# Performance work log

Measured on AMD Instinct MI355X. Metric: run time of the kernel, lower is better.

The kernel has to match this reference:

```python
import jax, jax.numpy as jnp
import numpy as np

N, E = 50000, 800000
IN_DIM, HID, OUT, HEADS = 128, 128, 64, 4
C1 = HID // HEADS  # 32 per-head channels in gat1
NEG_SLOPE = 0.2


def _gat_conv(x, src, dst, W, a_src, a_dst, b, heads, ch):
    """PyG GATConv (inference): gather -> edge attention -> segment softmax -> scatter."""
    n = x.shape[0]
    h = (x @ W).reshape(n, heads, ch)                      # [N,H,C]
    alpha_src = jnp.einsum('nhc,hc->nh', h, a_src)         # [N,H]
    alpha_dst = jnp.einsum('nhc,hc->nh', h, a_dst)         # [N,H]
    e = jax.nn.leaky_relu(alpha_src[src] + alpha_dst[dst], NEG_SLOPE)  # [E,H]
    m = jax.ops.segment_max(e, dst, num_segments=n)        # per-target max (stable softmax)
    e = jnp.exp(e - m[dst])
    denom = jax.ops.segment_sum(e, dst, num_segments=n)
    alpha = e / (denom[dst] + 1e-16)                       # [E,H]
    out = jax.ops.segment_sum(h[src] * alpha[:, :, None], dst, num_segments=n)  # [N,H,C]
    return out.reshape(n, heads * ch) + b


def setup_inputs() -> dict:
    key = jax.random.key(0)
    ks = jax.random.split(key, 16)
    x = jax.random.normal(ks[0], (N, IN_DIM), dtype=jnp.float32)
    edge_index = jax.random.randint(ks[1], (2, E), 0, N, dtype=jnp.int64)
    s = lambda fan_in: 1.0 / np.sqrt(fan_in)
    return {
        'x': x,
        'edge_index': edge_index,
        'W1': jax.random.normal(ks[2], (IN_DIM, HEADS * C1), jnp.float32) * s(IN_DIM),
        'a_src1': jax.random.normal(ks[3], (HEADS, C1), jnp.float32) * s(C1),
        'a_dst1': jax.random.normal(ks[4], (HEADS, C1), jnp.float32) * s(C1),
        'b1': jnp.zeros((HID,), jnp.float32),
        'W2': jax.random.normal(ks[5], (HID, OUT), jnp.float32) * s(HID),
        'a_src2': jax.random.normal(ks[6], (1, OUT), jnp.float32) * s(OUT),
        'a_dst2': jax.random.normal(ks[7], (1, OUT), jnp.float32) * s(OUT),
        'b2': jnp.zeros((OUT,), jnp.float32),
        'pw1': jax.random.normal(ks[8], (OUT, OUT), jnp.float32) * s(OUT),
        'pb1': jnp.zeros((OUT,), jnp.float32),
        'pw2': jax.random.normal(ks[9], (OUT, OUT), jnp.float32) * s(OUT),
        'pb2': jnp.zeros((OUT,), jnp.float32),
    }


def reference(x, edge_index, W1, a_src1, a_dst1, b1, W2, a_src2, a_dst2, b2, pw1, pb1, pw2, pb2):
    n = x.shape[0]
    # PyG GATConv add_self_loops=True
    loops = jnp.arange(n, dtype=edge_index.dtype)
    src = jnp.concatenate([edge_index[0], loops])
    dst = jnp.concatenate([edge_index[1], loops])
    h = jax.nn.elu(_gat_conv(x, src, dst, W1, a_src1, a_dst1, b1, HEADS, C1))
    h = jax.nn.elu(_gat_conv(h, src, dst, W2, a_src2, a_dst2, b2, 1, OUT))
    # origin_proj: Linear -> ReLU -> Linear
    h = jax.nn.relu(h @ pw1 + pb1)
    return h @ pw2 + pb2
```

## Files before the change

### kernel.cpp

```cpp
#include <hip/hip_runtime.h>
#include <math.h>

#define N_NODES 50000
#define N_EDGES 800000
#define ET (N_EDGES + N_NODES)
#define IN_DIM 128
#define HID 128
#define OUT_DIM 64
#define BW 64
#define NBUCK ((N_NODES + BW - 1) / BW)
#define NBLK 256
#define EPB 3328

__device__ __forceinline__ float lrelu(float x){ return x >= 0.f ? x : 0.2f * x; }
__device__ __forceinline__ float eluf(float x){ return x > 0.f ? x : expm1f(x); }
__device__ __forceinline__ unsigned f2bf(float f){
    unsigned u = __float_as_uint(f);
    return (u + 0x7fffu + ((u >> 16) & 1u)) >> 16;
}
__device__ __forceinline__ float bflo(unsigned u){ return __uint_as_float(u << 16); }
__device__ __forceinline__ float bfhi(unsigned u){ return __uint_as_float(u & 0xffff0000u); }

__global__ __launch_bounds__(256) void k_count(const int* __restrict__ dst, int* __restrict__ C)
{
    __shared__ int cnt[NBUCK];
    const int tid = threadIdx.x, blk = blockIdx.x;
    for (int i = tid; i < NBUCK; i += 256) cnt[i] = 0;
    __syncthreads();
    #pragma unroll
    for (int j = 0; j < EPB / 256; j++) {
        const int e = blk * EPB + j * 256 + tid;
        if (e < ET) {
            const int d = (e < N_EDGES) ? dst[e] : (e - N_EDGES);
            atomicAdd(&cnt[d >> 6], 1);
        }
    }
    __syncthreads();
    for (int b = tid; b < NBUCK; b += 256) C[b * NBLK + blk] = cnt[b];
}

__global__ __launch_bounds__(256) void k_bsumA(const int* __restrict__ C, int* __restrict__ bsum2)
{
    __shared__ int red[4];
    int v = C[blockIdx.x * NBLK + threadIdx.x];
    #pragma unroll
    for (int off = 32; off > 0; off >>= 1) v += __shfl_down(v, off);
    if ((threadIdx.x & 63) == 0) red[threadIdx.x >> 6] = v;
    __syncthreads();
    if (threadIdx.x == 0) bsum2[blockIdx.x] = red[0] + red[1] + red[2] + red[3];
}

__global__ __launch_bounds__(1024) void k_bscanB(const int* __restrict__ bsum2, int* __restrict__ boff2)
{
    __shared__ int part[1024];
    const int t = threadIdx.x;
    int v = (t < NBUCK) ? bsum2[t] : 0;
    part[t] = v;
    __syncthreads();
    #pragma unroll
    for (int d = 1; d < 1024; d <<= 1) {
        int add = (t >= d) ? part[t - d] : 0;
        __syncthreads();
        part[t] += add;
        __syncthreads();
    }
    if (t < NBUCK) boff2[t] = part[t] - v;
    if (t == 0) boff2[NBUCK] = ET;
}

__global__ __launch_bounds__(256) void k_cscanC(const int* __restrict__ C,
                                                const int* __restrict__ boff2,
                                                int* __restrict__ Cs)
{
    __shared__ int part[256];
    const int t = threadIdx.x, b = blockIdx.x;
    int v = C[b * NBLK + t];
    part[t] = v;
    __syncthreads();
    #pragma unroll
    for (int d = 1; d < 256; d <<= 1) {
        int add = (t >= d) ? part[t - d] : 0;
        __syncthreads();
        part[t] += add;
        __syncthreads();
    }
    Cs[b * NBLK + t] = boff2[b] + part[t] - v;
}

__global__ __launch_bounds__(256) void k_part2(const int* __restrict__ src,
                                               const int* __restrict__ dst,
                                               const int* __restrict__ Cs,
                                               uint2* __restrict__ part)
{
    __shared__ int base[NBUCK];
    __shared__ int cnt[NBUCK];
    const int tid = threadIdx.x, blk = blockIdx.x;
    for (int b = tid; b < NBUCK; b += 256) { base[b] = Cs[b * NBLK + blk]; cnt[b] = 0; }
    __syncthreads();
    #pragma unroll
    for (int j = 0; j < EPB / 256; j++) {
        const int e = blk * EPB + j * 256 + tid;
        if (e < ET) {
            int s, d;
            if (e < N_EDGES) { s = src[e]; d = dst[e]; } else { s = d = e - N_EDGES; }
            const int b = d >> 6;
            const int r = atomicAdd(&cnt[b], 1);
            part[base[b] + r] = make_uint2((unsigned)d, (unsigned)s);
        }
    }
}

__global__ __launch_bounds__(256) void k_scat2(const int* __restrict__ boff2,
                                               const uint2* __restrict__ part,
                                               int* __restrict__ rowptr,
                                               int* __restrict__ csr_src)
{
    __shared__ int cnt64[BW];
    __shared__ int nbase[BW];
    const int b = blockIdx.x, tid = threadIdx.x;
    const int n0 = b * BW;
    const int lo = boff2[b], hi = boff2[b + 1];
    if (tid < BW) cnt64[tid] = 0;
    __syncthreads();
    for (int i = lo + tid; i < hi; i += 256) {
        atomicAdd(&cnt64[part[i].x & (BW - 1)], 1);
    }
    __syncthreads();
    if (tid < BW) {
        int v = cnt64[tid];
        int incl = v;
        #pragma unroll
        for (int off = 1; off < 64; off <<= 1) {
            int t2 = __shfl_up(incl, off);
            if (tid >= off) incl += t2;
        }
        const int excl = incl - v;
        nbase[tid] = excl;
        const int n = n0 + tid;
        if (n < N_NODES) rowptr[n] = lo + excl;
        cnt64[tid] = 0;
    }
    if (b == 0 && tid == 0) rowptr[N_NODES] = ET;
    __syncthreads();
    for (int i = lo + tid; i < hi; i += 256) {
        const uint2 p = part[i];
        const int dn = (int)p.x & (BW - 1);
        const int r = atomicAdd(&cnt64[dn], 1);
        csr_src[lo + nbase[dn] + r] = (int)p.y;
    }
}

__global__ __launch_bounds__(256, 2) void k_gemm1(
    const float* __restrict__ x, const float* __restrict__ W1,
    const float* __restrict__ a_s, const float* __restrict__ a_d,
    unsigned* __restrict__ h1b, float* __restrict__ as1, float* __restrict__ ad1)
{
    __shared__ float sW[128 * 128];
    __shared__ float sx[32][128];
    const int tid = threadIdx.x;
    for (int i = tid; i < 4096; i += 256) ((float4*)sW)[i] = ((const float4*)W1)[i];
    const int cg = tid & 31;
    const int ng = tid >> 5;
    const float4 as4 = ((const float4*)a_s)[cg];
    const float4 ad4 = ((const float4*)a_d)[cg];
    const int nGroups = (N_NODES + 31) / 32;
    for (int g = blockIdx.x; g < nGroups; g += gridDim.x) {
        const int n0 = g * 32;
        __syncthreads();
        #pragma unroll
        for (int j = 0; j < 4; j++) {
            const int i = tid + 256 * j;
            const int node = i >> 5, quad = i & 31;
            const int n = n0 + node;
            float4 v = make_float4(0.f, 0.f, 0.f, 0.f);
            if (n < N_NODES) v = ((const float4*)x)[n * 32 + quad];
            *(float4*)&sx[node][4 * quad] = v;
        }
        __syncthreads();
        float4 acc[4];
        #pragma unroll
        for (int m = 0; m < 4; m++) acc[m] = make_float4(0.f, 0.f, 0.f, 0.f);
        #pragma unroll 8
        for (int k = 0; k < 128; k++) {
            const float4 w = *(const float4*)&sW[k * 128 + 4 * cg];
            #pragma unroll
            for (int m = 0; m < 4; m++) {
                const float xv = sx[4 * ng + m][k];
                acc[m].x = fmaf(xv, w.x, acc[m].x);
                acc[m].y = fmaf(xv, w.y, acc[m].y);
                acc[m].z = fmaf(xv, w.z, acc[m].z);
                acc[m].w = fmaf(xv, w.w, acc[m].w);
            }
        }
        #pragma unroll
        for (int m = 0; m < 4; m++) {
            const int n = n0 + 4 * ng + m;
            float ps = acc[m].x * as4.x + acc[m].y * as4.y + acc[m].z * as4.z + acc[m].w * as4.w;
            float pd = acc[m].x * ad4.x + acc[m].y * ad4.y + acc[m].z * ad4.z + acc[m].w * ad4.w;
            #pragma unroll
            for (int off = 1; off < 8; off <<= 1) {
                ps += __shfl_xor(ps, off);
                pd += __shfl_xor(pd, off);
            }
            if (n < N_NODES) {
                uint2 pk;
                pk.x = f2bf(acc[m].x) | (f2bf(acc[m].y) << 16);
                pk.y = f2bf(acc[m].z) | (f2bf(acc[m].w) << 16);
                ((uint2*)h1b)[n * 32 + cg] = pk;
                if ((cg & 7) == 0) {
                    as1[n * 4 + (cg >> 3)] = ps;
                    ad1[n * 4 + (cg >> 3)] = pd;
                }
            }
        }
    }
}

__global__ __launch_bounds__(256) void k_aggr1(
    const int* __restrict__ rowptr, const int* __restrict__ csr_src,
    const float* __restrict__ as1, const float* __restrict__ ad1,
    const uint4* __restrict__ h1u4, float* __restrict__ acc1)
{
    const int d  = blockIdx.x * 16 + (threadIdx.x >> 4);
    const int c8 = threadIdx.x & 15;
    const int hd = c8 >> 2;
    const int r0 = rowptr[d], r1 = rowptr[d + 1];
    const float adv = ad1[d * 4 + hd];
    float den = 0.f;
    float acc[8];
    #pragma unroll
    for (int m = 0; m < 8; m++) acc[m] = 0.f;
    int i = r0;
    for (; i + 2 <= r1; i += 2) {
        const int s0 = csr_src[i], s1 = csr_src[i + 1];
        const float e0 = as1[s0 * 4 + hd], e1 = as1[s1 * 4 + hd];
        const uint4 u0 = h1u4[s0 * 16 + c8];
        const uint4 u1 = h1u4[s1 * 16 + c8];
        const float w0 = expf(lrelu(e0 + adv));
        const float w1 = expf(lrelu(e1 + adv));
        den += w0 + w1;
        acc[0] = fmaf(bflo(u0.x), w0, acc[0]); acc[1] = fmaf(bfhi(u0.x), w0, acc[1]);
        acc[2] = fmaf(bflo(u0.y), w0, acc[2]); acc[3] = fmaf(bfhi(u0.y), w0, acc[3]);
        acc[4] = fmaf(bflo(u0.z), w0, acc[4]); acc[5] = fmaf(bfhi(u0.z), w0, acc[5]);
        acc[6] = fmaf(bflo(u0.w), w0, acc[6]); acc[7] = fmaf(bfhi(u0.w), w0, acc[7]);
        acc[0] = fmaf(bflo(u1.x), w1, acc[0]); acc[1] = fmaf(bfhi(u1.x), w1, acc[1]);
        acc[2] = fmaf(bflo(u1.y), w1, acc[2]); acc[3] = fmaf(bfhi(u1.y), w1, acc[3]);
        acc[4] = fmaf(bflo(u1.z), w1, acc[4]); acc[5] = fmaf(bfhi(u1.z), w1, acc[5]);
        acc[6] = fmaf(bflo(u1.w), w1, acc[6]); acc[7] = fmaf(bfhi(u1.w), w1, acc[7]);
    }
    if (i < r1) {
        const int s = csr_src[i];
        const float w = expf(lrelu(as1[s * 4 + hd] + adv));
        const uint4 u = h1u4[s * 16 + c8];
        den += w;
        acc[0] = fmaf(bflo(u.x), w, acc[0]); acc[1] = fmaf(bfhi(u.x), w, acc[1]);
        acc[2] = fmaf(bflo(u.y), w, acc[2]); acc[3] = fmaf(bfhi(u.y), w, acc[3]);
        acc[4] = fmaf(bflo(u.z), w, acc[4]); acc[5] = fmaf(bfhi(u.z), w, acc[5]);
        acc[6] = fmaf(bflo(u.w), w, acc[6]); acc[7] = fmaf(bfhi(u.w), w, acc[7]);
    }
    const float inv = 1.f / (den + 1e-16f);
    float4 o0 = make_float4(acc[0] * inv, acc[1] * inv, acc[2] * inv, acc[3] * inv);
    float4 o1 = make_float4(acc[4] * inv, acc[5] * inv, acc[6] * inv, acc[7] * inv);
    ((float4*)acc1)[d * 32 + 2 * c8 + 0] = o0;
    ((float4*)acc1)[d * 32 + 2 * c8 + 1] = o1;
}

__global__ __launch_bounds__(256, 2) void k_layer2(
    const float* __restrict__ acc1, const float* __restrict__ b1,
    const float* __restrict__ W2, const float* __restrict__ a_s2, const float* __restrict__ a_d2,
    unsigned* __restrict__ h2b, float* __restrict__ as2, float* __restrict__ ad2)
{
    __shared__ float sW[128 * 64];
    __shared__ float sh[64][132];
    const int tid = threadIdx.x;
    for (int i = tid; i < 2048; i += 256) ((float4*)sW)[i] = ((const float4*)W2)[i];
    const int cg = tid & 15;
    const int ng = tid >> 4;
    const float4 as4 = ((const float4*)a_s2)[cg];
    const float4 ad4 = ((const float4*)a_d2)[cg];
    const int nGroups = (N_NODES + 63) / 64;
    for (int g = blockIdx.x; g < nGroups; g += gridDim.x) {
        const int n0 = g * 64;
        __syncthreads();
        #pragma unroll
        for (int j = 0; j < 8; j++) {
            const int i = tid + 256 * j;
            const int node = i >> 5, quad = i & 31;
            const int n = n0 + node;
            float4 v = make_float4(0.f, 0.f, 0.f, 0.f);
            if (n < N_NODES) {
                v = ((const float4*)acc1)[n * 32 + quad];
                const float4 bb = ((const float4*)b1)[quad];
                v.x = eluf(v.x + bb.x);
                v.y = eluf(v.y + bb.y);
                v.z = eluf(v.z + bb.z);
                v.w = eluf(v.w + bb.w);
            }
            *(float4*)&sh[node][4 * quad] = v;
        }
        __syncthreads();
        float4 acc[4];
        #pragma unroll
        for (int m = 0; m < 4; m++) acc[m] = make_float4(0.f, 0.f, 0.f, 0.f);
        #pragma unroll 8
        for (int k = 0; k < 128; k++) {
            const float4 w = *(const float4*)&sW[k * 64 + 4 * cg];
            #pragma unroll
            for (int m = 0; m < 4; m++) {
                const float xv = sh[4 * ng + m][k];
                acc[m].x = fmaf(xv, w.x, acc[m].x);
                acc[m].y = fmaf(xv, w.y, acc[m].y);
                acc[m].z = fmaf(xv, w.z, acc[m].z);
                acc[m].w = fmaf(xv, w.w, acc[m].w);
            }
        }
        #pragma unroll
        for (int m = 0; m < 4; m++) {
            const int n = n0 + 4 * ng + m;
            float ps = acc[m].x * as4.x + acc[m].y * as4.y + acc[m].z * as4.z + acc[m].w * as4.w;
            float pd = acc[m].x * ad4.x + acc[m].y * ad4.y + acc[m].z * ad4.z + acc[m].w * ad4.w;
            #pragma unroll
            for (int off = 1; off < 16; off <<= 1) {
                ps += __shfl_xor(ps, off);
                pd += __shfl_xor(pd, off);
            }
            if (n < N_NODES) {
                uint2 pk;
                pk.x = f2bf(acc[m].x) | (f2bf(acc[m].y) << 16);
                pk.y = f2bf(acc[m].z) | (f2bf(acc[m].w) << 16);
                ((uint2*)h2b)[n * 16 + cg] = pk;
                if (cg == 0) { as2[n] = ps; ad2[n] = pd; }
            }
        }
    }
}

__global__ __launch_bounds__(256) void k_aggr2(
    const int* __restrict__ rowptr, const int* __restrict__ csr_src,
    const float* __restrict__ as2, const float* __restrict__ ad2,
    const uint4* __restrict__ h2u4, float* __restrict__ acc2)
{
    const int d  = blockIdx.x * 32 + (threadIdx.x >> 3);
    const int c8 = threadIdx.x & 7;
    if (d >= N_NODES) return;
    const int r0 = rowptr[d], r1 = rowptr[d + 1];
    const float adv = ad2[d];
    float den = 0.f;
    float acc[8];
    #pragma unroll
    for (int m = 0; m < 8; m++) acc[m] = 0.f;
    int i = r0;
    for (; i + 2 <= r1; i += 2) {
        const int s0 = csr_src[i], s1 = csr_src[i + 1];
        const float e0 = as2[s0], e1 = as2[s1];
        const uint4 u0 = h2u4[s0 * 8 + c8];
        const uint4 u1 = h2u4[s1 * 8 + c8];
        const float w0 = expf(lrelu(e0 + adv));
        const float w1 = expf(lrelu(e1 + adv));
        den += w0 + w1;
        acc[0] = fmaf(bflo(u0.x), w0, acc[0]); acc[1] = fmaf(bfhi(u0.x), w0, acc[1]);
        acc[2] = fmaf(bflo(u0.y), w0, acc[2]); acc[3] = fmaf(bfhi(u0.y), w0, acc[3]);
        acc[4] = fmaf(bflo(u0.z), w0, acc[4]); acc[5] = fmaf(bfhi(u0.z), w0, acc[5]);
        acc[6] = fmaf(bflo(u0.w), w0, acc[6]); acc[7] = fmaf(bfhi(u0.w), w0, acc[7]);
        acc[0] = fmaf(bflo(u1.x), w1, acc[0]); acc[1] = fmaf(bfhi(u1.x), w1, acc[1]);
        acc[2] = fmaf(bflo(u1.y), w1, acc[2]); acc[3] = fmaf(bfhi(u1.y), w1, acc[3]);
        acc[4] = fmaf(bflo(u1.z), w1, acc[4]); acc[5] = fmaf(bfhi(u1.z), w1, acc[5]);
        acc[6] = fmaf(bflo(u1.w), w1, acc[6]); acc[7] = fmaf(bfhi(u1.w), w1, acc[7]);
    }
    if (i < r1) {
        const int s = csr_src[i];
        const float w = expf(lrelu(as2[s] + adv));
        const uint4 u = h2u4[s * 8 + c8];
        den += w;
        acc[0] = fmaf(bflo(u.x), w, acc[0]); acc[1] = fmaf(bfhi(u.x), w, acc[1]);
        acc[2] = fmaf(bflo(u.y), w, acc[2]); acc[3] = fmaf(bfhi(u.y), w, acc[3]);
        acc[4] = fmaf(bflo(u.z), w, acc[4]); acc[5] = fmaf(bfhi(u.z), w, acc[5]);
        acc[6] = fmaf(bflo(u.w), w, acc[6]); acc[7] = fmaf(bfhi(u.w), w, acc[7]);
    }
    const float inv = 1.f / (den + 1e-16f);
    float4 o0 = make_float4(acc[0] * inv, acc[1] * inv, acc[2] * inv, acc[3] * inv);
    float4 o1 = make_float4(acc[4] * inv, acc[5] * inv, acc[6] * inv, acc[7] * inv);
    ((float4*)acc2)[d * 16 + 2 * c8 + 0] = o0;
    ((float4*)acc2)[d * 16 + 2 * c8 + 1] = o1;
}

__global__ __launch_bounds__(256, 2) void k_out(
    const float* __restrict__ acc2, const float* __restrict__ b2,
    const float* __restrict__ pw1, const float* __restrict__ pb1,
    const float* __restrict__ pw2, const float* __restrict__ pb2,
    float* __restrict__ out)
{
    __shared__ float s1[64 * 64];
    __shared__ float s2[64 * 64];
    __shared__ float so[64][68];
    __shared__ float sp[64][68];
    const int tid = threadIdx.x;
    for (int i = tid; i < 1024; i += 256) {
        ((float4*)s1)[i] = ((const float4*)pw1)[i];
        ((float4*)s2)[i] = ((const float4*)pw2)[i];
    }
    const int cg = tid & 15;
    const int ng = tid >> 4;
    const float4 pb1_4 = ((const float4*)pb1)[cg];
    const float4 pb2_4 = ((const float4*)pb2)[cg];
    const int nGroups = (N_NODES + 63) / 64;
    for (int g = blockIdx.x; g < nGroups; g += gridDim.x) {
        const int n0 = g * 64;
        __syncthreads();
        #pragma unroll
        for (int j = 0; j < 4; j++) {
            const int i = tid + 256 * j;
            const int node = i >> 4, quad = i & 15;
            const int n = n0 + node;
            float4 v = make_float4(0.f, 0.f, 0.f, 0.f);
            if (n < N_NODES) {
                v = ((const float4*)acc2)[n * 16 + quad];
                const float4 bb = ((const float4*)b2)[quad];
                v.x = eluf(v.x + bb.x);
                v.y = eluf(v.y + bb.y);
                v.z = eluf(v.z + bb.z);
                v.w = eluf(v.w + bb.w);
            }
            *(float4*)&so[node][4 * quad] = v;
        }
        __syncthreads();
        float4 p[4];
        #pragma unroll
        for (int m = 0; m < 4; m++) p[m] = pb1_4;
        #pragma unroll 8
        for (int k = 0; k < 64; k++) {
            const float4 w = *(const float4*)&s1[k * 64 + 4 * cg];
            #pragma unroll
            for (int m = 0; m < 4; m++) {
                const float xv = so[4 * ng + m][k];
                p[m].x = fmaf(xv, w.x, p[m].x);
                p[m].y = fmaf(xv, w.y, p[m].y);
                p[m].z = fmaf(xv, w.z, p[m].z);
                p[m].w = fmaf(xv, w.w, p[m].w);
            }
        }
        #pragma unroll
        for (int m = 0; m < 4; m++) {
            p[m].x = fmaxf(p[m].x, 0.f); p[m].y = fmaxf(p[m].y, 0.f);
            p[m].z = fmaxf(p[m].z, 0.f); p[m].w = fmaxf(p[m].w, 0.f);
            *(float4*)&sp[4 * ng + m][4 * cg] = p[m];
        }
        __syncthreads();
        float4 o[4];
        #pragma unroll
        for (int m = 0; m < 4; m++) o[m] = pb2_4;
        #pragma unroll 8
        for (int k = 0; k < 64; k++) {
            const float4 w = *(const float4*)&s2[k * 64 + 4 * cg];
            #pragma unroll
            for (int m = 0; m < 4; m++) {
                const float xv = sp[4 * ng + m][k];
                o[m].x = fmaf(xv, w.x, o[m].x);
                o[m].y = fmaf(xv, w.y, o[m].y);
                o[m].z = fmaf(xv, w.z, o[m].z);
                o[m].w = fmaf(xv, w.w, o[m].w);
            }
        }
        #pragma unroll
        for (int m = 0; m < 4; m++) {
            const int n = n0 + 4 * ng + m;
            if (n < N_NODES) ((float4*)out)[n * 16 + cg] = o[m];
        }
    }
}

extern "C" void kernel_launch(void* const* d_in, const int* in_sizes, int n_in,
                              void* d_out, int out_size, void* d_ws, size_t ws_size,
                              hipStream_t stream)
{
    const float* x      = (const float*)d_in[0];
    const int*   ei     = (const int*)d_in[1];
    const int*   src    = ei;
    const int*   dst    = ei + N_EDGES;
    const float* W1     = (const float*)d_in[2];
    const float* a_src1 = (const float*)d_in[3];
    const float* a_dst1 = (const float*)d_in[4];
    const float* b1     = (const float*)d_in[5];
    const float* W2     = (const float*)d_in[6];
    const float* a_src2 = (const float*)d_in[7];
    const float* a_dst2 = (const float*)d_in[8];
    const float* b2     = (const float*)d_in[9];
    const float* pw1    = (const float*)d_in[10];
    const float* pb1    = (const float*)d_in[11];
    const float* pw2    = (const float*)d_in[12];
    const float* pb2    = (const float*)d_in[13];

    uint2* part  = (uint2*)d_ws;
    int* ibase   = (int*)(part + ET);
    int* rowptr  = ibase;
    int* C       = rowptr + 50001;
    int* Cs      = C + 200192;
    int* bsum2   = Cs + 200192;
    int* boff2   = bsum2 + 782;
    int* csr_src = boff2 + 785;
    unsigned* h1b = (unsigned*)(csr_src + 850000);
    unsigned* h2b = h1b + 3200000;
    float* fws   = (float*)(h2b + 1600000);
    float* as1   = fws;
    float* ad1   = as1 + 200000;
    float* acc1  = ad1 + 200000;
    float* as2   = acc1 + 6400000;
    float* ad2   = as2 + 50000;
    float* acc2  = ad2 + 50000;

    k_count<<<NBLK, 256, 0, stream>>>(dst, C);
    k_bsumA<<<NBUCK, 256, 0, stream>>>(C, bsum2);
    k_bscanB<<<1, 1024, 0, stream>>>(bsum2, boff2);
    k_cscanC<<<NBUCK, 256, 0, stream>>>(C, boff2, Cs);
    k_part2<<<NBLK, 256, 0, stream>>>(src, dst, Cs, part);
    k_scat2<<<NBUCK, 256, 0, stream>>>(boff2, part, rowptr, csr_src);

    k_gemm1<<<1563, 256, 0, stream>>>(x, W1, a_src1, a_dst1, h1b, as1, ad1);
    k_aggr1<<<N_NODES / 16, 256, 0, stream>>>(rowptr, csr_src, as1, ad1,
                                              (const uint4*)h1b, acc1);

    k_layer2<<<782, 256, 0, stream>>>(acc1, b1, W2, a_src2, a_dst2, h2b, as2, ad2);
    k_aggr2<<<(N_NODES + 31) / 32, 256, 0, stream>>>(rowptr, csr_src, as2, ad2,
                                                     (const uint4*)h2b, acc2);

    k_out<<<782, 256, 0, stream>>>(acc2, b2, pw1, pb1, pw2, pb2, (float*)d_out);
}
```

Before: 274.5 us.

## Retile node GEMMs with K-chunked shared tiles and 8x8 register blocking

```diff
diff --git a/kernel.cpp b/kernel.cpp
--- a/kernel.cpp
+++ b/kernel.cpp
@@ -150,67 +150,96 @@
     }
 }
 
-__global__ __launch_bounds__(256, 2) void k_gemm1(
+__global__ __launch_bounds__(256, 3) void k_gemm1(
     const float* __restrict__ x, const float* __restrict__ W1,
     const float* __restrict__ a_s, const float* __restrict__ a_d,
     unsigned* __restrict__ h1b, float* __restrict__ as1, float* __restrict__ ad1)
 {
-    __shared__ float sW[128 * 128];
-    __shared__ float sx[32][128];
+    __shared__ float sW[32 * 128];
+    __shared__ float sx[128 * 32];
+    float4* sW4 = (float4*)sW;
+    float4* sx4 = (float4*)sx;
+    const float4* x4  = (const float4*)x;
+    const float4* W14 = (const float4*)W1;
     const int tid = threadIdx.x;
-    for (int i = tid; i < 4096; i += 256) ((float4*)sW)[i] = ((const float4*)W1)[i];
-    const int cg = tid & 31;
-    const int ng = tid >> 5;
-    const float4 as4 = ((const float4*)a_s)[cg];
-    const float4 ad4 = ((const float4*)a_d)[cg];
-    const int nGroups = (N_NODES + 31) / 32;
-    for (int g = blockIdx.x; g < nGroups; g += gridDim.x) {
-        const int n0 = g * 32;
+    const int cg = tid & 15;
+    const int ng = tid >> 4;
+    const int axor = ng & 7;
+    const int n0 = blockIdx.x * 128;
+
+    float4 acc[8][2];
+    #pragma unroll
+    for (int m = 0; m < 8; m++) { acc[m][0] = make_float4(0,0,0,0); acc[m][1] = make_float4(0,0,0,0); }
+
+    for (int c = 0; c < 4; c++) {
         __syncthreads();
         #pragma unroll
         for (int j = 0; j < 4; j++) {
-            const int i = tid + 256 * j;
-            const int node = i >> 5, quad = i & 31;
+            const int idx = tid + 256 * j;
+            float4 v = W14[c * 1024 + idx];
+            const int k = idx >> 5, f = idx & 31;
+            sW4[k * 32 + ((f & 1) << 4) + (f >> 1)] = v;
+        }
+        #pragma unroll
+        for (int j = 0; j < 4; j++) {
+            const int idx = tid + 256 * j;
+            const int node = idx >> 3, q = idx & 7;
             const int n = n0 + node;
-            float4 v = make_float4(0.f, 0.f, 0.f, 0.f);
-            if (n < N_NODES) v = ((const float4*)x)[n * 32 + quad];
-            *(float4*)&sx[node][4 * quad] = v;
-        }
-        __syncthreads();
-        float4 acc[4];
-        #pragma unroll
-        for (int m = 0; m < 4; m++) acc[m] = make_float4(0.f, 0.f, 0.f, 0.f);
-        #pragma unroll 8
-        for (int k = 0; k < 128; k++) {
-            const float4 w = *(const float4*)&sW[k * 128 + 4 * cg];
-            #pragma unroll
-            for (int m = 0; m < 4; m++) {
-                const float xv = sx[4 * ng + m][k];
-                acc[m].x = fmaf(xv, w.x, acc[m].x);
-                acc[m].y = fmaf(xv, w.y, acc[m].y);
-                acc[m].z = fmaf(xv, w.z, acc[m].z);
-                acc[m].w = fmaf(xv, w.w, acc[m].w);
-            }
-        }
-        #pragma unroll
-        for (int m = 0; m < 4; m++) {
-            const int n = n0 + 4 * ng + m;
-            float ps = acc[m].x * as4.x + acc[m].y * as4.y + acc[m].z * as4.z + acc[m].w * as4.w;
-            float pd = acc[m].x * ad4.x + acc[m].y * ad4.y + acc[m].z * ad4.z + acc[m].w * ad4.w;
-            #pragma unroll
-            for (int off = 1; off < 8; off <<= 1) {
-                ps += __shfl_xor(ps, off);
-                pd += __shfl_xor(pd, off);
-            }
-            if (n < N_NODES) {
-                uint2 pk;
-                pk.x = f2bf(acc[m].x) | (f2bf(acc[m].y) << 16);
-                pk.y = f2bf(acc[m].z) | (f2bf(acc[m].w) << 16);
-                ((uint2*)h1b)[n * 32 + cg] = pk;
-                if ((cg & 7) == 0) {
-                    as1[n * 4 + (cg >> 3)] = ps;
-                    ad1[n * 4 + (cg >> 3)] = pd;
-                }
+            float4 v = make_float4(0,0,0,0);
+            if (n < N_NODES) v = x4[n * 32 + c * 8 + q];
+            sx4[node * 8 + (q ^ ((node >> 3) & 7))] = v;
+        }
+        __syncthreads();
+        #pragma unroll 2
+        for (int k4 = 0; k4 < 8; k4++) {
+            float4 w0[4], w1[4];
+            #pragma unroll
+            for (int ks = 0; ks < 4; ks++) {
+                w0[ks] = sW4[(4 * k4 + ks) * 32 + cg];
+                w1[ks] = sW4[(4 * k4 + ks) * 32 + 16 + cg];
+            }
+            float4 xv[8];
+            #pragma unroll
+            for (int m = 0; m < 8; m++) xv[m] = sx4[(8 * ng + m) * 8 + (k4 ^ axor)];
+            #pragma unroll
+            for (int m = 0; m < 8; m++) {
+                const float4 xm = xv[m];
+                #define FMA8(S, KS) \
+                    acc[m][0].x = fmaf(S, w0[KS].x, acc[m][0].x); \
+                    acc[m][0].y = fmaf(S, w0[KS].y, acc[m][0].y); \
+                    acc[m][0].z = fmaf(S, w0[KS].z, acc[m][0].z); \
+                    acc[m][0].w = fmaf(S, w0[KS].w, acc[m][0].w); \
+                    acc[m][1].x = fmaf(S, w1[KS].x, acc[m][1].x); \
+                    acc[m][1].y = fmaf(S, w1[KS].y, acc[m][1].y); \
+                    acc[m][1].z = fmaf(S, w1[KS].z, acc[m][1].z); \
+                    acc[m][1].w = fmaf(S, w1[KS].w, acc[m][1].w);
+                FMA8(xm.x, 0) FMA8(xm.y, 1) FMA8(xm.z, 2) FMA8(xm.w, 3)
+                #undef FMA8
+            }
+        }
+    }
+
+    const float4 as_a = ((const float4*)a_s)[2 * cg], as_b = ((const float4*)a_s)[2 * cg + 1];
+    const float4 ad_a = ((const float4*)a_d)[2 * cg], ad_b = ((const float4*)a_d)[2 * cg + 1];
+    #pragma unroll
+    for (int m = 0; m < 8; m++) {
+        const int n = n0 + 8 * ng + m;
+        float ps = acc[m][0].x * as_a.x + acc[m][0].y * as_a.y + acc[m][0].z * as_a.z + acc[m][0].w * as_a.w
+                 + acc[m][1].x * as_b.x + acc[m][1].y * as_b.y + acc[m][1].z * as_b.z + acc[m][1].w * as_b.w;
+        float pd = acc[m][0].x * ad_a.x + acc[m][0].y * ad_a.y + acc[m][0].z * ad_a.z + acc[m][0].w * ad_a.w
+                 + acc[m][1].x * ad_b.x + acc[m][1].y * ad_b.y + acc[m][1].z * ad_b.z + acc[m][1].w * ad_b.w;
+        ps += __shfl_xor(ps, 1); ps += __shfl_xor(ps, 2);
+        pd += __shfl_xor(pd, 1); pd += __shfl_xor(pd, 2);
+        if (n < N_NODES) {
+            uint4 pk;
+            pk.x = f2bf(acc[m][0].x) | (f2bf(acc[m][0].y) << 16);
+            pk.y = f2bf(acc[m][0].z) | (f2bf(acc[m][0].w) << 16);
+            pk.z = f2bf(acc[m][1].x) | (f2bf(acc[m][1].y) << 16);
+            pk.w = f2bf(acc[m][1].z) | (f2bf(acc[m][1].w) << 16);
+            ((uint4*)h1b)[n * 16 + cg] = pk;
+            if ((cg & 3) == 0) {
+                as1[n * 4 + (cg >> 2)] = ps;
+                ad1[n * 4 + (cg >> 2)] = pd;
             }
         }
     }
@@ -265,72 +294,102 @@
     ((float4*)acc1)[d * 32 + 2 * c8 + 1] = o1;
 }
 
-__global__ __launch_bounds__(256, 2) void k_layer2(
+__global__ __launch_bounds__(256, 3) void k_layer2(
     const float* __restrict__ acc1, const float* __restrict__ b1,
     const float* __restrict__ W2, const float* __restrict__ a_s2, const float* __restrict__ a_d2,
     unsigned* __restrict__ h2b, float* __restrict__ as2, float* __restrict__ ad2)
 {
-    __shared__ float sW[128 * 64];
-    __shared__ float sh[64][132];
+    __shared__ float sW[32 * 64];
+    __shared__ float sx[256 * 32];
+    float4* sW4 = (float4*)sW;
+    float4* sx4 = (float4*)sx;
+    const float4* a14 = (const float4*)acc1;
+    const float4* W24 = (const float4*)W2;
+    const float4* b14 = (const float4*)b1;
     const int tid = threadIdx.x;
-    for (int i = tid; i < 2048; i += 256) ((float4*)sW)[i] = ((const float4*)W2)[i];
-    const int cg = tid & 15;
-    const int ng = tid >> 4;
-    const float4 as4 = ((const float4*)a_s2)[cg];
-    const float4 ad4 = ((const float4*)a_d2)[cg];
-    const int nGroups = (N_NODES + 63) / 64;
-    for (int g = blockIdx.x; g < nGroups; g += gridDim.x) {
-        const int n0 = g * 64;
-        __syncthreads();
+    const int cg = tid & 7;
+    const int ng = tid >> 3;
+    const int axor = ng & 7;
+    const int n0 = blockIdx.x * 256;
+
+    float4 acc[8][2];
+    #pragma unroll
+    for (int m = 0; m < 8; m++) { acc[m][0] = make_float4(0,0,0,0); acc[m][1] = make_float4(0,0,0,0); }
+
+    for (int c = 0; c < 4; c++) {
+        __syncthreads();
+        #pragma unroll
+        for (int j = 0; j < 2; j++) {
+            const int idx = tid + 256 * j;
+            float4 v = W24[c * 512 + idx];
+            const int k = idx >> 4, f = idx & 15;
+            sW4[k * 16 + ((f & 1) << 3) + (f >> 1)] = v;
+        }
         #pragma unroll
         for (int j = 0; j < 8; j++) {
-            const int i = tid + 256 * j;
-            const int node = i >> 5, quad = i & 31;
+            const int idx = tid + 256 * j;
+            const int node = idx >> 3, q = idx & 7;
             const int n = n0 + node;
-            float4 v = make_float4(0.f, 0.f, 0.f, 0.f);
+            float4 v = make_float4(0,0,0,0);
             if (n < N_NODES) {
-                v = ((const float4*)acc1)[n * 32 + quad];
-                const float4 bb = ((const float4*)b1)[quad];
+                v = a14[n * 32 + c * 8 + q];
+                const float4 bb = b14[c * 8 + q];
                 v.x = eluf(v.x + bb.x);
                 v.y = eluf(v.y + bb.y);
                 v.z = eluf(v.z + bb.z);
                 v.w = eluf(v.w + bb.w);
             }
-            *(float4*)&sh[node][4 * quad] = v;
-        }
-        __syncthreads();
-        float4 acc[4];
-        #pragma unroll
-        for (int m = 0; m < 4; m++) acc[m] = make_float4(0.f, 0.f, 0.f, 0.f);
-        #pragma unroll 8
-        for (int k = 0; k < 128; k++) {
-            const float4 w = *(const float4*)&sW[k * 64 + 4 * cg];
-            #pragma unroll
-            for (int m = 0; m < 4; m++) {
-                const float xv = sh[4 * ng + m][k];
-                acc[m].x = fmaf(xv, w.x, acc[m].x);
-                acc[m].y = fmaf(xv, w.y, acc[m].y);
-                acc[m].z = fmaf(xv, w.z, acc[m].z);
-                acc[m].w = fmaf(xv, w.w, acc[m].w);
-            }
-        }
-        #pragma unroll
-        for (int m = 0; m < 4; m++) {
-            const int n = n0 + 4 * ng + m;
-            float ps = acc[m].x * as4.x + acc[m].y * as4.y + acc[m].z * as4.z + acc[m].w * as4.w;
-            float pd = acc[m].x * ad4.x + acc[m].y * ad4.y + acc[m].z * ad4.z + acc[m].w * ad4.w;
-            #pragma unroll
-            for (int off = 1; off < 16; off <<= 1) {
-                ps += __shfl_xor(ps, off);
-                pd += __shfl_xor(pd, off);
-            }
-            if (n < N_NODES) {
-                uint2 pk;
-                pk.x = f2bf(acc[m].x) | (f2bf(acc[m].y) << 16);
-                pk.y = f2bf(acc[m].z) | (f2bf(acc[m].w) << 16);
-                ((uint2*)h2b)[n * 16 + cg] = pk;
-                if (cg == 0) { as2[n] = ps; ad2[n] = pd; }
-            }
+            sx4[node * 8 + (q ^ ((node >> 3) & 7))] = v;
+        }
+        __syncthreads();
+        #pragma unroll 2
+        for (int k4 = 0; k4 < 8; k4++) {
+            float4 w0[4], w1[4];
+            #pragma unroll
+            for (int ks = 0; ks < 4; ks++) {
+                w0[ks] = sW4[(4 * k4 + ks) * 16 + cg];
+                w1[ks] = sW4[(4 * k4 + ks) * 16 + 8 + cg];
+            }
+            float4 xv[8];
+            #pragma unroll
+            for (int m = 0; m < 8; m++) xv[m] = sx4[(8 * ng + m) * 8 + (k4 ^ axor)];
+            #pragma unroll
+            for (int m = 0; m < 8; m++) {
+                const float4 xm = xv[m];
+                #define FMA8(S, KS) \
+                    acc[m][0].x = fmaf(S, w0[KS].x, acc[m][0].x); \
+                    acc[m][0].y = fmaf(S, w0[KS].y, acc[m][0].y); \
+                    acc[m][0].z = fmaf(S, w0[KS].z, acc[m][0].z); \
+                    acc[m][0].w = fmaf(S, w0[KS].w, acc[m][0].w); \
+                    acc[m][1].x = fmaf(S, w1[KS].x, acc[m][1].x); \
+                    acc[m][1].y = fmaf(S, w1[KS].y, acc[m][1].y); \
+                    acc[m][1].z = fmaf(S, w1[KS].z, acc[m][1].z); \
+                    acc[m][1].w = fmaf(S, w1[KS].w, acc[m][1].w);
+                FMA8(xm.x, 0) FMA8(xm.y, 1) FMA8(xm.z, 2) FMA8(xm.w, 3)
+                #undef FMA8
+            }
+        }
+    }
+
+    const float4 as_a = ((const float4*)a_s2)[2 * cg], as_b = ((const float4*)a_s2)[2 * cg + 1];
+    const float4 ad_a = ((const float4*)a_d2)[2 * cg], ad_b = ((const float4*)a_d2)[2 * cg + 1];
+    #pragma unroll
+    for (int m = 0; m < 8; m++) {
+        const int n = n0 + 8 * ng + m;
+        float ps = acc[m][0].x * as_a.x + acc[m][0].y * as_a.y + acc[m][0].z * as_a.z + acc[m][0].w * as_a.w
+                 + acc[m][1].x * as_b.x + acc[m][1].y * as_b.y + acc[m][1].z * as_b.z + acc[m][1].w * as_b.w;
+        float pd = acc[m][0].x * ad_a.x + acc[m][0].y * ad_a.y + acc[m][0].z * ad_a.z + acc[m][0].w * ad_a.w
+                 + acc[m][1].x * ad_b.x + acc[m][1].y * ad_b.y + acc[m][1].z * ad_b.z + acc[m][1].w * ad_b.w;
+        ps += __shfl_xor(ps, 1); ps += __shfl_xor(ps, 2); ps += __shfl_xor(ps, 4);
+        pd += __shfl_xor(pd, 1); pd += __shfl_xor(pd, 2); pd += __shfl_xor(pd, 4);
+        if (n < N_NODES) {
+            uint4 pk;
+            pk.x = f2bf(acc[m][0].x) | (f2bf(acc[m][0].y) << 16);
+            pk.y = f2bf(acc[m][0].z) | (f2bf(acc[m][0].w) << 16);
+            pk.z = f2bf(acc[m][1].x) | (f2bf(acc[m][1].y) << 16);
+            pk.w = f2bf(acc[m][1].z) | (f2bf(acc[m][1].w) << 16);
+            ((uint4*)h2b)[n * 8 + cg] = pk;
+            if (cg == 0) { as2[n] = ps; ad2[n] = pd; }
         }
     }
 }
@@ -515,11 +574,11 @@
     k_part2<<<NBLK, 256, 0, stream>>>(src, dst, Cs, part);
     k_scat2<<<NBUCK, 256, 0, stream>>>(boff2, part, rowptr, csr_src);
 
-    k_gemm1<<<1563, 256, 0, stream>>>(x, W1, a_src1, a_dst1, h1b, as1, ad1);
+    k_gemm1<<<(N_NODES + 127) / 128, 256, 0, stream>>>(x, W1, a_src1, a_dst1, h1b, as1, ad1);
     k_aggr1<<<N_NODES / 16, 256, 0, stream>>>(rowptr, csr_src, as1, ad1,
                                               (const uint4*)h1b, acc1);
 
-    k_layer2<<<782, 256, 0, stream>>>(acc1, b1, W2, a_src2, a_dst2, h2b, as2, ad2);
+    k_layer2<<<(N_NODES + 255) / 256, 256, 0, stream>>>(acc1, b1, W2, a_src2, a_dst2, h2b, as2, ad2);
     k_aggr2<<<(N_NODES + 31) / 32, 256, 0, stream>>>(rowptr, csr_src, as2, ad2,
                                                      (const uint4*)h2b, acc2);
 
```

Result: no change. 277.2 us (+1.0%).
